# Kernel optimization log

Measured on AMD Instinct MI355X. Metric: run time of the kernel, lower is better.

## Reference

```python
import jax, jax.numpy as jnp
import numpy as np

VOCAB, EMB, HID = 32000, 128, 256
B, S = 16, 512


def setup_inputs() -> dict:
    key = jax.random.key(0)
    ks = jax.random.split(key, 8)
    sc = 0.05
    return {
        "x": jax.random.randint(ks[0], (B, S), 0, VOCAB),
        "emb_table": jax.random.normal(ks[1], (VOCAB, EMB), jnp.float32) * sc,
        "w_ih": jax.random.normal(ks[2], (4 * HID, EMB), jnp.float32) * sc,
        "w_hh": jax.random.normal(ks[3], (4 * HID, HID), jnp.float32) * sc,
        "b_ih": jax.random.normal(ks[4], (4 * HID,), jnp.float32) * sc,
        "b_hh": jax.random.normal(ks[5], (4 * HID,), jnp.float32) * sc,
        "w_out": jax.random.normal(ks[6], (VOCAB, HID), jnp.float32) * sc,
        "b_out": jax.random.normal(ks[7], (VOCAB,), jnp.float32) * sc,
    }


def _lstm(emb, w_ih, w_hh, b_ih, b_hh):
    # emb: [B, S, E]. Precompute input contribution for all timesteps.
    xg = jnp.einsum("bse,ge->bsg", emb, w_ih) + (b_ih + b_hh)  # [B, S, 4H]
    xg = jnp.transpose(xg, (1, 0, 2))  # [S, B, 4H] for scan over time
    H = w_hh.shape[1]
    h0 = jnp.zeros((emb.shape[0], H), emb.dtype)
    c0 = jnp.zeros_like(h0)

    def step(carry, xg_t):
        h, c = carry
        gates = xg_t + h @ w_hh.T  # [B, 4H]
        i, f, g, o = jnp.split(gates, 4, axis=-1)  # torch gate order i,f,g,o
        i = jax.nn.sigmoid(i)
        f = jax.nn.sigmoid(f)
        g = jnp.tanh(g)
        o = jax.nn.sigmoid(o)
        c_new = f * c + i * g
        h_new = o * jnp.tanh(c_new)
        return (h_new, c_new), h_new

    _, hs = jax.lax.scan(step, (h0, c0), xg)  # hs: [S, B, H]
    return jnp.transpose(hs, (1, 0, 2))  # [B, S, H]


def reference(x, emb_table, w_ih, w_hh, b_ih, b_hh, w_out, b_out):
    emb = emb_table[x]  # [B, S, E] embedding lookup
    h = _lstm(emb, w_ih, w_hh, b_ih, b_hh)  # [B, S, H]
    logits = jnp.einsum("bsh,vh->bsv", h, w_out) + b_out  # [B, S, V]
    return logits
```

## Files before the change

kernel.cpp:

```cpp
#include <hip/hip_runtime.h>


typedef __bf16 v8bf __attribute__((ext_vector_type(8)));
typedef __bf16 v4bf __attribute__((ext_vector_type(4)));
typedef float  v4f  __attribute__((ext_vector_type(4)));

#define BATCH 16
#define SEQ   512
#define EMB   128
#define HID   256
#define G4H   1024
#define VOCAB 32000
#define MROWS (BATCH*SEQ)

__device__ __forceinline__ float fast_sigmoid(float x) {
    float e = __builtin_amdgcn_exp2f(-1.442695040888963f * x);
    return __builtin_amdgcn_rcpf(1.0f + e);
}
__device__ __forceinline__ float fast_tanh(float x) {
    float e = __builtin_amdgcn_exp2f(-2.885390081777927f * x);
    return 2.0f * __builtin_amdgcn_rcpf(1.0f + e) - 1.0f;
}

__global__ void cvt_kernel(const float* __restrict__ in, __bf16* __restrict__ out, int n4) {
    int i = blockIdx.x * blockDim.x + threadIdx.x;
    if (i < n4) {
        float4 v = ((const float4*)in)[i];
        v4bf p;
        p[0] = (__bf16)v.x; p[1] = (__bf16)v.y; p[2] = (__bf16)v.z; p[3] = (__bf16)v.w;
        ((v4bf*)out)[i] = p;
    }
}

template<bool GATHER, bool PERMUTE>
__global__ __launch_bounds__(256)
void gemm_kernel(const __bf16* __restrict__ A, const __bf16* __restrict__ B,
                 const float* __restrict__ bias1, const float* __restrict__ bias2,
                 float* __restrict__ out, int K, int ldout,
                 const int* __restrict__ xidx, const float* __restrict__ emb)
{
    __shared__ __bf16 Al[128 * 40];
    __shared__ __bf16 Bl[128 * 40];

    const int tid  = threadIdx.x;
    const int w    = tid >> 6, l = tid & 63;
    const int m    = l & 15, quad = l >> 4;
    const int wm   = w >> 1, wn = w & 1;
    const int row0 = blockIdx.y * 128;
    const int col0 = blockIdx.x * 128;

    v4f acc[4][4];
    #pragma unroll
    for (int i = 0; i < 4; ++i)
        #pragma unroll
        for (int j = 0; j < 4; ++j) {
            v4f z = {0.f, 0.f, 0.f, 0.f};
            acc[i][j] = z;
        }

    for (int k0 = 0; k0 < K; k0 += 32) {
        if (GATHER) {
            #pragma unroll
            for (int it = 0; it < 4; ++it) {
                int e = it * 256 + tid;
                int r = e >> 3, sg = e & 7;
                int mr = row0 + r;
                int idx = xidx[(mr & 15) * SEQ + (mr >> 4)];
                float4 v = *(const float4*)(emb + (size_t)idx * EMB + k0 + sg * 4);
                v4bf p;
                p[0] = (__bf16)v.x; p[1] = (__bf16)v.y; p[2] = (__bf16)v.z; p[3] = (__bf16)v.w;
                *(v4bf*)&Al[r * 40 + sg * 4] = p;
            }
        } else {
            #pragma unroll
            for (int it = 0; it < 2; ++it) {
                int e = it * 256 + tid;
                int r = e >> 2, sg = e & 3;
                int4 v = *(const int4*)(A + (size_t)(row0 + r) * K + k0 + sg * 8);
                *(int4*)&Al[r * 40 + sg * 8] = v;
            }
        }
        #pragma unroll
        for (int it = 0; it < 2; ++it) {
            int e = it * 256 + tid;
            int r = e >> 2, sg = e & 3;
            int4 v = *(const int4*)(B + (size_t)(col0 + r) * K + k0 + sg * 8);
            *(int4*)&Bl[r * 40 + sg * 8] = v;
        }
        __syncthreads();

        v8bf af[4], bfr[4];
        #pragma unroll
        for (int i = 0; i < 4; ++i)
            af[i] = *(const v8bf*)&Al[(wm * 64 + i * 16 + m) * 40 + quad * 8];
        #pragma unroll
        for (int j = 0; j < 4; ++j)
            bfr[j] = *(const v8bf*)&Bl[(wn * 64 + j * 16 + m) * 40 + quad * 8];

        #pragma unroll
        for (int i = 0; i < 4; ++i)
            #pragma unroll
            for (int j = 0; j < 4; ++j)
                acc[i][j] = __builtin_amdgcn_mfma_f32_16x16x32_bf16(af[i], bfr[j], acc[i][j], 0, 0, 0);
        __syncthreads();
    }

    #pragma unroll
    for (int j = 0; j < 4; ++j) {
        int colg = col0 + wn * 64 + j * 16 + m;
        float bs = bias1[colg];
        if (bias2) bs += bias2[colg];
        #pragma unroll
        for (int i = 0; i < 4; ++i) {
            #pragma unroll
            for (int r = 0; r < 4; ++r) {
                int rg = row0 + wm * 64 + i * 16 + quad * 4 + r;
                size_t orow = PERMUTE ? (size_t)((rg & 15) * SEQ + (rg >> 4)) : (size_t)rg;
                out[orow * (size_t)ldout + colg] = acc[i][j][r] + bs;
            }
        }
    }
}

__global__ __launch_bounds__(1024)
void lstm_kernel(const float* __restrict__ xg, const float* __restrict__ w_hh,
                 __bf16* __restrict__ hs)
{
    __shared__ __bf16 h_lds[4096];

    const int tid  = threadIdx.x;
    const int w    = tid >> 6;
    const int l    = tid & 63;
    const int m    = l & 15;
    const int quad = l >> 4;

    v8bf bw[4][8];
    #pragma unroll
    for (int q = 0; q < 4; ++q)
        #pragma unroll
        for (int s = 0; s < 8; ++s) {
            const float* src = w_hh + (size_t)(q * 256 + w * 16 + m) * HID + s * 32 + quad * 8;
            float4 v0 = *(const float4*)(src);
            float4 v1 = *(const float4*)(src + 4);
            v8bf f;
            f[0] = (__bf16)v0.x; f[1] = (__bf16)v0.y; f[2] = (__bf16)v0.z; f[3] = (__bf16)v0.w;
            f[4] = (__bf16)v1.x; f[5] = (__bf16)v1.y; f[6] = (__bf16)v1.z; f[7] = (__bf16)v1.w;
            bw[q][s] = f;
        }

    for (int i = tid; i < 4096; i += 1024) h_lds[i] = (__bf16)0.0f;

    float c0[4] = {0.f, 0.f, 0.f, 0.f};

    float xgc[16];
    #pragma unroll
    for (int q = 0; q < 4; ++q)
        #pragma unroll
        for (int r = 0; r < 4; ++r)
            xgc[q * 4 + r] = xg[(size_t)(quad * 4 + r) * G4H + q * 256 + w * 16 + m];

    __syncthreads();

    for (int t = 0; t < SEQ; ++t) {
        v8bf af[8];
        #pragma unroll
        for (int s = 0; s < 8; ++s)
            af[s] = *(const v8bf*)&h_lds[s * 512 + l * 8];
        __syncthreads();

        float xgn[16];
        {
            int tn = (t < SEQ - 1) ? t + 1 : t;
            const float* xgt = xg + (size_t)tn * BATCH * G4H;
            #pragma unroll
            for (int q = 0; q < 4; ++q)
                #pragma unroll
                for (int r = 0; r < 4; ++r)
                    xgn[q * 4 + r] = xgt[(size_t)(quad * 4 + r) * G4H + q * 256 + w * 16 + m];
        }

        v4f accq[4];
        #pragma unroll
        for (int q = 0; q < 4; ++q) {
            v4f acc;
            #pragma unroll
            for (int r = 0; r < 4; ++r) acc[r] = xgc[q * 4 + r];
            #pragma unroll
            for (int s = 0; s < 8; ++s)
                acc = __builtin_amdgcn_mfma_f32_16x16x32_bf16(af[s], bw[q][s], acc, 0, 0, 0);
            accq[q] = acc;
        }

        #pragma unroll
        for (int r = 0; r < 4; ++r) {
            float i_ = fast_sigmoid(accq[0][r]);
            float f_ = fast_sigmoid(accq[1][r]);
            float g_ = fast_tanh(accq[2][r]);
            float o_ = fast_sigmoid(accq[3][r]);
            float c  = f_ * c0[r] + i_ * g_;
            c0[r] = c;
            float h = o_ * fast_tanh(c);

            int b = quad * 4 + r;
            int k = w * 16 + m;
            __bf16 hb = (__bf16)h;
            h_lds[(k >> 3) * 128 + b * 8 + (k & 7)] = hb;
            hs[(size_t)(t * 16 + b) * HID + k] = hb;
        }
        __syncthreads();

        #pragma unroll
        for (int i = 0; i < 16; ++i) xgc[i] = xgn[i];
    }
}

extern "C" void kernel_launch(void* const* d_in, const int* in_sizes, int n_in,
                              void* d_out, int out_size, void* d_ws, size_t ws_size,
                              hipStream_t stream) {
    const int*   x     = (const int*)d_in[0];
    const float* emb   = (const float*)d_in[1];
    const float* w_ih  = (const float*)d_in[2];
    const float* w_hh  = (const float*)d_in[3];
    const float* b_ih  = (const float*)d_in[4];
    const float* b_hh  = (const float*)d_in[5];
    const float* w_out = (const float*)d_in[6];
    const float* b_out = (const float*)d_in[7];
    float* out = (float*)d_out;

    char* ws = (char*)d_ws;
    float*  xgbuf = (float*)(ws);
    __bf16* hsbuf = (__bf16*)(ws + 33554432);
    __bf16* wihb  = (__bf16*)(ws + 37748736);
    __bf16* woutb = (__bf16*)(ws + 38010880);

    cvt_kernel<<<(G4H * EMB / 4 + 255) / 256, 256, 0, stream>>>(w_ih, wihb, G4H * EMB / 4);
    cvt_kernel<<<(VOCAB * HID / 4 + 255) / 256, 256, 0, stream>>>(w_out, woutb, VOCAB * HID / 4);

    gemm_kernel<true, false><<<dim3(G4H / 128, MROWS / 128), 256, 0, stream>>>(
        nullptr, wihb, b_ih, b_hh, xgbuf, EMB, G4H, x, emb);

    lstm_kernel<<<1, 1024, 0, stream>>>(xgbuf, w_hh, hsbuf);

    gemm_kernel<false, true><<<dim3(VOCAB / 128, MROWS / 128), 256, 0, stream>>>(
        hsbuf, woutb, b_out, nullptr, out, HID, VOCAB, nullptr, nullptr);
}
```

Before: 5.579 ms.

## Fuse input projection into LSTM recurrence and double-buffer hidden state

Removes the separate input-projection GEMM and its fp32 gate buffer. A small prep kernel now gathers embeddings into a bf16 MFMA-ready layout, and the single-block LSTM kernel computes the x·W_ih contribution with extra MFMAs each step, holding W_ih fragments in registers. The hidden state in LDS is double-buffered, which drops one barrier per step, and the global hs store is moved after the barrier. The output GEMM also gets an XCD-aware workgroup swizzle. The cost is more MFMAs and higher register pressure inside the serial recurrence, which sits on the critical path.

New measurement: 8.637 ms. 54.8% more time.

```diff
diff --git a/kernel.cpp b/kernel.cpp
--- a/kernel.cpp
+++ b/kernel.cpp
@@ -30,6 +30,24 @@
         p[0] = (__bf16)v.x; p[1] = (__bf16)v.y; p[2] = (__bf16)v.z; p[3] = (__bf16)v.w;
         ((v4bf*)out)[i] = p;
     }
+}
+
+__global__ __launch_bounds__(256)
+void xe_prep_kernel(const int* __restrict__ x, const float* __restrict__ emb,
+                    __bf16* __restrict__ xe)
+{
+    int t   = blockIdx.x;
+    int tid = threadIdx.x;
+    int b = tid >> 4, kk = tid & 15;
+    int idx = x[b * SEQ + t];
+    const float* src = emb + (size_t)idx * EMB + kk * 8;
+    float4 v0 = *(const float4*)src;
+    float4 v1 = *(const float4*)(src + 4);
+    v8bf p;
+    p[0] = (__bf16)v0.x; p[1] = (__bf16)v0.y; p[2] = (__bf16)v0.z; p[3] = (__bf16)v0.w;
+    p[4] = (__bf16)v1.x; p[5] = (__bf16)v1.y; p[6] = (__bf16)v1.z; p[7] = (__bf16)v1.w;
+    int s = kk >> 2, quad = kk & 3;
+    *(v8bf*)&xe[(size_t)t * 2048 + s * 512 + (quad * 16 + b) * 8] = p;
 }
 
 template<bool GATHER, bool PERMUTE>
@@ -46,8 +64,20 @@
     const int w    = tid >> 6, l = tid & 63;
     const int m    = l & 15, quad = l >> 4;
     const int wm   = w >> 1, wn = w & 1;
-    const int row0 = blockIdx.y * 128;
-    const int col0 = blockIdx.x * 128;
+
+    int bxi = blockIdx.x, byi = blockIdx.y;
+    {
+        int nwg = gridDim.x * gridDim.y;
+        if ((nwg & 7) == 0) {
+            int wg  = byi * gridDim.x + bxi;
+            int cpx = nwg >> 3;
+            int swz = (wg & 7) * cpx + (wg >> 3);
+            bxi = swz % gridDim.x;
+            byi = swz / gridDim.x;
+        }
+    }
+    const int row0 = byi * 128;
+    const int col0 = bxi * 128;
 
     v4f acc[4][4];
     #pragma unroll
@@ -123,10 +153,11 @@
 }
 
 __global__ __launch_bounds__(1024)
-void lstm_kernel(const float* __restrict__ xg, const float* __restrict__ w_hh,
-                 __bf16* __restrict__ hs)
+void lstm_kernel(const __bf16* __restrict__ xe, const __bf16* __restrict__ wih,
+                 const float* __restrict__ w_hh, const float* __restrict__ b_ih,
+                 const float* __restrict__ b_hh, __bf16* __restrict__ hs)
 {
-    __shared__ __bf16 h_lds[4096];
+    __shared__ __align__(16) __bf16 h_lds[2][4096];
 
     const int tid  = threadIdx.x;
     const int w    = tid >> 6;
@@ -148,49 +179,61 @@
             bw[q][s] = f;
         }
 
-    for (int i = tid; i < 4096; i += 1024) h_lds[i] = (__bf16)0.0f;
+    v8bf bx[4][4];
+    #pragma unroll
+    for (int q = 0; q < 4; ++q)
+        #pragma unroll
+        for (int s = 0; s < 4; ++s)
+            bx[q][s] = *(const v8bf*)&wih[(size_t)(q * 256 + w * 16 + m) * EMB + s * 32 + quad * 8];
+
+    float bs4[4];
+    #pragma unroll
+    for (int q = 0; q < 4; ++q) {
+        int col = q * 256 + w * 16 + m;
+        bs4[q] = b_ih[col] + b_hh[col];
+    }
+
+    for (int i = tid; i < 4096; i += 1024) h_lds[0][i] = (__bf16)0.0f;
 
     float c0[4] = {0.f, 0.f, 0.f, 0.f};
 
-    float xgc[16];
-    #pragma unroll
-    for (int q = 0; q < 4; ++q)
-        #pragma unroll
-        for (int r = 0; r < 4; ++r)
-            xgc[q * 4 + r] = xg[(size_t)(quad * 4 + r) * G4H + q * 256 + w * 16 + m];
-
     __syncthreads();
 
+    const int k      = w * 16 + m;
+    const int hw_off = (k >> 3) * 128 + (k & 7);
+
     for (int t = 0; t < SEQ; ++t) {
-        v8bf af[8];
-        #pragma unroll
-        for (int s = 0; s < 8; ++s)
-            af[s] = *(const v8bf*)&h_lds[s * 512 + l * 8];
-        __syncthreads();
-
-        float xgn[16];
-        {
-            int tn = (t < SEQ - 1) ? t + 1 : t;
-            const float* xgt = xg + (size_t)tn * BATCH * G4H;
+        const __bf16* xet = xe + (size_t)t * 2048;
+        v8bf xf[4];
+        #pragma unroll
+        for (int s = 0; s < 4; ++s)
+            xf[s] = *(const v8bf*)&xet[s * 512 + l * 8];
+
+        const __bf16* hb = h_lds[t & 1];
+
+        v4f accq[4];
+        #pragma unroll
+        for (int q = 0; q < 4; ++q) {
+            v4f a;
+            a[0] = bs4[q]; a[1] = bs4[q]; a[2] = bs4[q]; a[3] = bs4[q];
+            accq[q] = a;
+        }
+
+        #pragma unroll
+        for (int s = 0; s < 8; ++s) {
+            v8bf af = *(const v8bf*)&hb[s * 512 + l * 8];
             #pragma unroll
             for (int q = 0; q < 4; ++q)
-                #pragma unroll
-                for (int r = 0; r < 4; ++r)
-                    xgn[q * 4 + r] = xgt[(size_t)(quad * 4 + r) * G4H + q * 256 + w * 16 + m];
-        }
-
-        v4f accq[4];
-        #pragma unroll
-        for (int q = 0; q < 4; ++q) {
-            v4f acc;
-            #pragma unroll
-            for (int r = 0; r < 4; ++r) acc[r] = xgc[q * 4 + r];
-            #pragma unroll
-            for (int s = 0; s < 8; ++s)
-                acc = __builtin_amdgcn_mfma_f32_16x16x32_bf16(af[s], bw[q][s], acc, 0, 0, 0);
-            accq[q] = acc;
-        }
-
+                accq[q] = __builtin_amdgcn_mfma_f32_16x16x32_bf16(af, bw[q][s], accq[q], 0, 0, 0);
+        }
+        #pragma unroll
+        for (int s = 0; s < 4; ++s)
+            #pragma unroll
+            for (int q = 0; q < 4; ++q)
+                accq[q] = __builtin_amdgcn_mfma_f32_16x16x32_bf16(xf[s], bx[q][s], accq[q], 0, 0, 0);
+
+        __bf16* hwv = h_lds[(t + 1) & 1];
+        __bf16 hreg[4];
         #pragma unroll
         for (int r = 0; r < 4; ++r) {
             float i_ = fast_sigmoid(accq[0][r]);
@@ -200,17 +243,15 @@
             float c  = f_ * c0[r] + i_ * g_;
             c0[r] = c;
             float h = o_ * fast_tanh(c);
-
-            int b = quad * 4 + r;
-            int k = w * 16 + m;
-            __bf16 hb = (__bf16)h;
-            h_lds[(k >> 3) * 128 + b * 8 + (k & 7)] = hb;
-            hs[(size_t)(t * 16 + b) * HID + k] = hb;
+            __bf16 hv = (__bf16)h;
+            hreg[r] = hv;
+            hwv[hw_off + (quad * 4 + r) * 8] = hv;
         }
         __syncthreads();
 
         #pragma unroll
-        for (int i = 0; i < 16; ++i) xgc[i] = xgn[i];
+        for (int r = 0; r < 4; ++r)
+            hs[(size_t)(t * 16 + quad * 4 + r) * HID + k] = hreg[r];
     }
 }
 
@@ -228,18 +269,16 @@
     float* out = (float*)d_out;
 
     char* ws = (char*)d_ws;
-    float*  xgbuf = (float*)(ws);
-    __bf16* hsbuf = (__bf16*)(ws + 33554432);
-    __bf16* wihb  = (__bf16*)(ws + 37748736);
-    __bf16* woutb = (__bf16*)(ws + 38010880);
+    __bf16* xebuf = (__bf16*)(ws);
+    __bf16* hsbuf = (__bf16*)(ws + 2097152);
+    __bf16* wihb  = (__bf16*)(ws + 6291456);
+    __bf16* woutb = (__bf16*)(ws + 6553600);
 
     cvt_kernel<<<(G4H * EMB / 4 + 255) / 256, 256, 0, stream>>>(w_ih, wihb, G4H * EMB / 4);
     cvt_kernel<<<(VOCAB * HID / 4 + 255) / 256, 256, 0, stream>>>(w_out, woutb, VOCAB * HID / 4);
-
-    gemm_kernel<true, false><<<dim3(G4H / 128, MROWS / 128), 256, 0, stream>>>(
-        nullptr, wihb, b_ih, b_hh, xgbuf, EMB, G4H, x, emb);
-
-    lstm_kernel<<<1, 1024, 0, stream>>>(xgbuf, w_hh, hsbuf);
+    xe_prep_kernel<<<SEQ, 256, 0, stream>>>(x, emb, xebuf);
+
+    lstm_kernel<<<1, 1024, 0, stream>>>(xebuf, wihb, w_hh, b_ih, b_hh, hsbuf);
 
     gemm_kernel<false, true><<<dim3(VOCAB / 128, MROWS / 128), 256, 0, stream>>>(
         hsbuf, woutb, b_out, nullptr, out, HID, VOCAB, nullptr, nullptr);
```
